# Optimization experiments

Hardware: AMD Instinct MI355X
Metric: run time of the kernel (lower is better)

## Reference

```python
import jax, jax.numpy as jnp
import numpy as np
import math

E = 64          # embed_size
S = 64          # max_seq_len (mask hard-codes seq==64)
H = 8           # num_heads
DH = E // H     # 8
DFF = 4 * E     # 256
V = 32000       # vocab_size
B = 64          # batch


def _pos_encoding():
    position = np.arange(0, S, dtype=np.float32)[:, None]
    div_term = np.exp(np.arange(0, E, 2, dtype=np.float32) * -(math.log(10000.0) / E))
    pe = np.zeros((S, E), dtype=np.float32)
    pe[:, 0::2] = np.sin(position * div_term)
    pe[:, 1::2] = np.cos(position * div_term)
    return jnp.asarray(pe)


def layernorm(x, g, b, eps=1e-5):
    mu = jnp.mean(x, -1, keepdims=True)
    var = jnp.mean((x - mu) ** 2, -1, keepdims=True)
    return (x - mu) * jax.lax.rsqrt(var + eps) * g + b


def round4(x):
    return jnp.round(x * 1e4) / 1e4


def setup_inputs() -> dict:
    key = jax.random.key(0)
    ks = jax.random.split(key, 16)
    n = lambda k, sh, s=0.05: jax.random.normal(k, sh, dtype=jnp.float32) * s
    return {
        "x": jax.random.randint(ks[0], (B, S), 0, V),
        "emb": n(ks[1], (V, E), 1.0),
        "pe": _pos_encoding(),
        # per-head q/k/v weights concatenated: [E, H*DH] == [E, E], no bias
        "wq": n(ks[2], (E, E)), "wk": n(ks[3], (E, E)), "wv": n(ks[4], (E, E)),
        "g_h": jnp.ones((E,)), "b_h": jnp.zeros((E,)),           # MHA internal LayerNorm
        "wo": n(ks[5], (E, E)), "bo": jnp.zeros((E,)),           # MHA output linear
        "g1": jnp.ones((E,)), "bt1": jnp.zeros((E,)),            # norm1
        "w1": n(ks[6], (E, DFF)), "b1f": jnp.zeros((DFF,)),      # ffn fc1
        "w2": n(ks[7], (DFF, E)), "b2f": jnp.zeros((E,)),        # ffn fc2
        "g2": jnp.ones((E,)), "bt2": jnp.zeros((E,)),            # norm2
        "gf": jnp.ones((E,)), "bf": jnp.zeros((E,)),             # final norm
        "wout": n(ks[8], (E, V)), "bout": jnp.zeros((V,)),       # final linear
    }


def reference(x, emb, pe, wq, wk, wv, g_h, b_h, wo, bo, g1, bt1,
              w1, b1f, w2, b2f, g2, bt2, gf, bf, wout, bout):
    # embedding + positional encoding (dropout = identity in eval)
    h = emb[x] + pe[:S]                              # [B,S,E]

    # --- multi-head attention (per-head linears fused as one GEMM each) ---
    q = (h @ wq).reshape(B, S, H, DH)
    k = (h @ wk).reshape(B, S, H, DH)
    v = (h @ wv).reshape(B, S, H, DH)
    scores = jnp.einsum('bshd,bthd->bhst', q, k) / math.sqrt(DH)
    causal = jnp.tril(jnp.ones((S, S), dtype=bool))
    scores = jnp.where(causal, scores, -jnp.inf)
    attn = jax.nn.softmax(scores, axis=-1)
    ho = round4(jnp.einsum('bhst,bthd->bshd', attn, v))  # per-head round(decimals=4)
    concat = ho.reshape(B, S, E)
    attn_out = jnp.round(layernorm(concat, g_h, b_h) @ wo + bo)  # round to integers

    # --- transformer block residual/norm/ffn ---
    h = layernorm(h + attn_out, g1, bt1)
    ffn = jax.nn.relu(h @ w1 + b1f) @ w2 + b2f
    h = round4(layernorm(h + ffn, g2, bt2))

    # --- final norm, vocab projection, softmax, round ---
    logits = layernorm(h, gf, bf) @ wout + bout       # [B,S,V]
    probs = jax.nn.softmax(logits, axis=-1)
    return jnp.round(probs)
```

## Files before the change

kernel.cpp:

```cpp
#include <hip/hip_runtime.h>
#include <hip/hip_bf16.h>
#include <math.h>

#define EMB 64
#define SEQ 64
#define NH 8
#define DFF 256
#define VOC 32000
#define BATCH 64

using bf16_t = __hip_bfloat16;
typedef __bf16 bf16x8 __attribute__((ext_vector_type(8)));
typedef float f32x4 __attribute__((ext_vector_type(4)));

#define WOUTT_OFF 0
#define HBF_OFF   4194304
#define GSUM_OFF  (4194304 + 524288)
#define GMAX_OFF  (GSUM_OFF + 16384)
#define H_OFF     (GMAX_OFF + 32768)
#define Q_OFF     (H_OFF + 1048576)
#define K_OFF     (Q_OFF + 1048576)
#define V_OFF     (K_OFF + 1048576)
#define HO_OFF    (V_OFF + 1048576)

#define NV_TOTAL 32768000
#define F1_BLKS 360
#define F1_PER  32000
#define F2_BLKS 192
#define F2_PER  30000
#define F3_BLKS 360
#define F3_PER  32000
#define F4_BLKS 64
#define F4_PER  62000
#define F2_BASE 11520000
#define F3_BASE 17280000
#define F4_BASE 28800000

__device__ inline void fill_slice(float* __restrict__ outp, size_t vbase, int count, int t) {
  f32x4 z = {0.f, 0.f, 0.f, 0.f};
  f32x4* o4 = (f32x4*)outp + vbase;
  for (int i = t; i < count; i += 256) o4[i] = z;
}

__device__ inline unsigned long long packmax(float f, int i) {
  unsigned u = __float_as_uint(f);
  u = (u & 0x80000000u) ? ~u : (u | 0x80000000u);
  return ((unsigned long long)u << 32) | (unsigned)i;
}

__device__ inline float rsum16(float s) {
  s += __shfl_xor(s, 1, 16);
  s += __shfl_xor(s, 2, 16);
  s += __shfl_xor(s, 4, 16);
  s += __shfl_xor(s, 8, 16);
  return s;
}

__device__ inline void gemm64g(const float* __restrict__ in, const float* __restrict__ W,
                               float* __restrict__ out, int t) {
  int i = t >> 2, j0 = (t & 3) * 16;
  float acc[16];
#pragma unroll
  for (int j = 0; j < 16; ++j) acc[j] = 0.f;
#pragma unroll 2
  for (int k = 0; k < 64; ++k) {
    float a = in[i * 65 + k];
    const float4* wr = (const float4*)(W + k * 64 + j0);
    float4 w0 = wr[0], w1v = wr[1], w2v = wr[2], w3v = wr[3];
    acc[0] += a * w0.x;   acc[1] += a * w0.y;   acc[2] += a * w0.z;   acc[3] += a * w0.w;
    acc[4] += a * w1v.x;  acc[5] += a * w1v.y;  acc[6] += a * w1v.z;  acc[7] += a * w1v.w;
    acc[8] += a * w2v.x;  acc[9] += a * w2v.y;  acc[10] += a * w2v.z; acc[11] += a * w2v.w;
    acc[12] += a * w3v.x; acc[13] += a * w3v.y; acc[14] += a * w3v.z; acc[15] += a * w3v.w;
  }
#pragma unroll
  for (int j = 0; j < 16; ++j) out[(size_t)i * 64 + j0 + j] = acc[j];
}

__global__ __launch_bounds__(256) void k_qkv(
    const int* __restrict__ x, const float* __restrict__ emb, const float* __restrict__ pe,
    const float* __restrict__ wq, const float* __restrict__ wk, const float* __restrict__ wv,
    const float* __restrict__ wout, bf16_t* __restrict__ woutT,
    float* __restrict__ H, float* __restrict__ Q, float* __restrict__ K,
    float* __restrict__ V, float* __restrict__ gsums,
    unsigned long long* __restrict__ gmax, float* __restrict__ outp) {
  const int t = threadIdx.x;
  __shared__ float sm[64 * 65];

  if (blockIdx.x >= 564) {
    fill_slice(outp, (size_t)(blockIdx.x - 564) * F1_PER, F1_PER, t);
    return;
  }

  if (blockIdx.x >= 64) {
    int v0 = (blockIdx.x - 64) * 64;
    for (int idx = t; idx < 4096; idx += 256) {
      int e = idx >> 6, c = idx & 63;
      sm[e * 65 + c] = wout[(size_t)e * VOC + v0 + c];
    }
    __syncthreads();
    for (int idx = t; idx < 4096; idx += 256) {
      int c = idx >> 6, e = idx & 63;
      woutT[(size_t)(v0 + c) * 64 + e] = __float2bfloat16(sm[e * 65 + c]);
    }
    return;
  }

  const int b = blockIdx.x;
  if (t < 64) {
    gsums[b * 64 + t] = 0.f;
    gmax[b * 64 + t] = 0ULL;
  }
  for (int idx = t; idx < 4096; idx += 256) {
    int i = idx >> 6, e = idx & 63;
    int tok = x[b * 64 + i];
    float v = emb[(size_t)tok * 64 + e] + pe[i * 64 + e];
    sm[i * 65 + e] = v;
    H[((size_t)b * 64 + i) * 64 + e] = v;
  }
  __syncthreads();
  gemm64g(sm, wq, Q + (size_t)b * 4096, t);
  gemm64g(sm, wk, K + (size_t)b * 4096, t);
  gemm64g(sm, wv, V + (size_t)b * 4096, t);
}

__global__ __launch_bounds__(256) void k_attn(const float* __restrict__ Q,
                                              const float* __restrict__ K,
                                              const float* __restrict__ V,
                                              float* __restrict__ HO,
                                              float* __restrict__ outp) {
  const int t = threadIdx.x;
  if (blockIdx.x >= 64) {
    int bid = (blockIdx.x - 64) * 8 + blockIdx.y;
    fill_slice(outp, (size_t)F2_BASE + (size_t)bid * F2_PER, F2_PER, t);
    return;
  }
  const int b = blockIdx.x, h = blockIdx.y;
  __shared__ float Qh[64 * 8], Kh[64 * 8], Vh[64 * 8];
  __shared__ float SC[64 * 65];
  const size_t base = (size_t)b * 4096 + h * 8;

  for (int idx = t; idx < 512; idx += 256) {
    int i = idx >> 3, d = idx & 7;
    Qh[i * 8 + d] = Q[base + (size_t)i * 64 + d];
    Kh[i * 8 + d] = K[base + (size_t)i * 64 + d];
    Vh[i * 8 + d] = V[base + (size_t)i * 64 + d];
  }
  __syncthreads();

  const float scale = 0.35355339059327373f;
  const int i = t >> 2, jb = t & 3;
  float qv[8];
#pragma unroll
  for (int d = 0; d < 8; ++d) qv[d] = Qh[i * 8 + d];

  float sv[16];
  float m = -INFINITY;
#pragma unroll
  for (int jj = 0; jj < 16; ++jj) {
    int j = jb * 16 + jj;
    float s;
    if (j <= i) {
      s = 0.f;
#pragma unroll
      for (int d = 0; d < 8; ++d) s += qv[d] * Kh[j * 8 + d];
      s *= scale;
    } else {
      s = -INFINITY;
    }
    sv[jj] = s;
    m = fmaxf(m, s);
  }
  m = fmaxf(m, __shfl_xor(m, 1, 4));
  m = fmaxf(m, __shfl_xor(m, 2, 4));
  float sum = 0.f;
#pragma unroll
  for (int jj = 0; jj < 16; ++jj) {
    float e2 = __expf(sv[jj] - m);
    sv[jj] = e2;
    sum += e2;
  }
  sum += __shfl_xor(sum, 1, 4);
  sum += __shfl_xor(sum, 2, 4);
  float inv = 1.f / sum;
#pragma unroll
  for (int jj = 0; jj < 16; ++jj) SC[i * 65 + jb * 16 + jj] = sv[jj] * inv;
  __syncthreads();

  for (int idx = t; idx < 512; idx += 256) {
    int ii = idx >> 3, d = idx & 7;
    float o = 0.f;
    for (int j = 0; j < 64; ++j) o += SC[ii * 65 + j] * Vh[j * 8 + d];
    HO[base + (size_t)ii * 64 + d] = rintf(o * 1e4f) / 1e4f;
  }
}

__global__ __launch_bounds__(256) void k_ffn(
    const float* __restrict__ H, const float* __restrict__ HO,
    const float* __restrict__ g_h, const float* __restrict__ b_h,
    const float* __restrict__ wo, const float* __restrict__ bo,
    const float* __restrict__ g1, const float* __restrict__ bt1,
    const float* __restrict__ w1, const float* __restrict__ b1f,
    const float* __restrict__ w2, const float* __restrict__ b2f,
    const float* __restrict__ g2, const float* __restrict__ bt2,
    const float* __restrict__ gf, const float* __restrict__ bf_,
    bf16_t* __restrict__ hbf, float* __restrict__ outp) {
  const int t = threadIdx.x;
  if (blockIdx.x >= 256) {
    fill_slice(outp, (size_t)F3_BASE + (size_t)(blockIdx.x - 256) * F3_PER, F3_PER, t);
    return;
  }
  const int r0 = blockIdx.x * 16;
  const int i = t >> 4, l = t & 15;
  const int e0 = l * 4;
  const size_t row = (size_t)(r0 + i) * 64;
  __shared__ float T1[16 * 65];
  __shared__ float T2[16 * 65];
  __shared__ float H1[16 * 65];
  __shared__ float M[16 * 260];

  {
    float4 hv = *(const float4*)(HO + row + e0);
    float mu = rsum16(hv.x + hv.y + hv.z + hv.w) * (1.f / 64.f);
    float d0 = hv.x - mu, d1 = hv.y - mu, d2 = hv.z - mu, d3 = hv.w - mu;
    float var = rsum16(d0 * d0 + d1 * d1 + d2 * d2 + d3 * d3) * (1.f / 64.f);
    float rs = rsqrtf(var + 1e-5f);
    T1[i * 65 + e0 + 0] = d0 * rs * g_h[e0 + 0] + b_h[e0 + 0];
    T1[i * 65 + e0 + 1] = d1 * rs * g_h[e0 + 1] + b_h[e0 + 1];
    T1[i * 65 + e0 + 2] = d2 * rs * g_h[e0 + 2] + b_h[e0 + 2];
    T1[i * 65 + e0 + 3] = d3 * rs * g_h[e0 + 3] + b_h[e0 + 3];
  }
  __syncthreads();

  {
    float a0 = 0.f, a1 = 0.f, a2 = 0.f, a3 = 0.f;
#pragma unroll 4
    for (int k = 0; k < 64; ++k) {
      float a = T1[i * 65 + k];
      float4 w = *(const float4*)(wo + (size_t)k * 64 + e0);
      a0 += a * w.x; a1 += a * w.y; a2 += a * w.z; a3 += a * w.w;
    }
    T2[i * 65 + e0 + 0] = rintf(a0 + bo[e0 + 0]);
    T2[i * 65 + e0 + 1] = rintf(a1 + bo[e0 + 1]);
    T2[i * 65 + e0 + 2] = rintf(a2 + bo[e0 + 2]);
    T2[i * 65 + e0 + 3] = rintf(a3 + bo[e0 + 3]);
  }
  __syncthreads();

  {
    float4 hh = *(const float4*)(H + row + e0);
    float x0 = hh.x + T2[i * 65 + e0 + 0];
    float x1 = hh.y + T2[i * 65 + e0 + 1];
    float x2 = hh.z + T2[i * 65 + e0 + 2];
    float x3 = hh.w + T2[i * 65 + e0 + 3];
    float mu = rsum16(x0 + x1 + x2 + x3) * (1.f / 64.f);
    float d0 = x0 - mu, d1 = x1 - mu, d2 = x2 - mu, d3 = x3 - mu;
    float var = rsum16(d0 * d0 + d1 * d1 + d2 * d2 + d3 * d3) * (1.f / 64.f);
    float rs = rsqrtf(var + 1e-5f);
    H1[i * 65 + e0 + 0] = d0 * rs * g1[e0 + 0] + bt1[e0 + 0];
    H1[i * 65 + e0 + 1] = d1 * rs * g1[e0 + 1] + bt1[e0 + 1];
    H1[i * 65 + e0 + 2] = d2 * rs * g1[e0 + 2] + bt1[e0 + 2];
    H1[i * 65 + e0 + 3] = d3 * rs * g1[e0 + 3] + bt1[e0 + 3];
  }
  __syncthreads();

  {
    const int j0 = l * 16;
    float acc[16];
#pragma unroll
    for (int j = 0; j < 16; ++j) acc[j] = 0.f;
#pragma unroll 2
    for (int k = 0; k < 64; ++k) {
      float a = H1[i * 65 + k];
      const float4* wr = (const float4*)(w1 + (size_t)k * 256 + j0);
      float4 w0 = wr[0], w1v = wr[1], w2v = wr[2], w3v = wr[3];
      acc[0] += a * w0.x;   acc[1] += a * w0.y;   acc[2] += a * w0.z;   acc[3] += a * w0.w;
      acc[4] += a * w1v.x;  acc[5] += a * w1v.y;  acc[6] += a * w1v.z;  acc[7] += a * w1v.w;
      acc[8] += a * w2v.x;  acc[9] += a * w2v.y;  acc[10] += a * w2v.z; acc[11] += a * w2v.w;
      acc[12] += a * w3v.x; acc[13] += a * w3v.y; acc[14] += a * w3v.z; acc[15] += a * w3v.w;
    }
#pragma unroll
    for (int j = 0; j < 16; ++j)
      M[i * 260 + j0 + j] = fmaxf(acc[j] + b1f[j0 + j], 0.f);
  }
  __syncthreads();

  float f0 = 0.f, f1 = 0.f, f2 = 0.f, f3 = 0.f;
  {
#pragma unroll 4
    for (int k = 0; k < 256; ++k) {
      float a = M[i * 260 + k];
      float4 w = *(const float4*)(w2 + (size_t)k * 64 + e0);
      f0 += a * w.x; f1 += a * w.y; f2 += a * w.z; f3 += a * w.w;
    }
    f0 += b2f[e0 + 0]; f1 += b2f[e0 + 1]; f2 += b2f[e0 + 2]; f3 += b2f[e0 + 3];
  }

  {
    float y0 = H1[i * 65 + e0 + 0] + f0;
    float y1 = H1[i * 65 + e0 + 1] + f1;
    float y2 = H1[i * 65 + e0 + 2] + f2;
    float y3 = H1[i * 65 + e0 + 3] + f3;
    float mu = rsum16(y0 + y1 + y2 + y3) * (1.f / 64.f);
    float d0 = y0 - mu, d1 = y1 - mu, d2 = y2 - mu, d3 = y3 - mu;
    float var = rsum16(d0 * d0 + d1 * d1 + d2 * d2 + d3 * d3) * (1.f / 64.f);
    float rs = rsqrtf(var + 1e-5f);
    float h20 = rintf((d0 * rs * g2[e0 + 0] + bt2[e0 + 0]) * 1e4f) / 1e4f;
    float h21 = rintf((d1 * rs * g2[e0 + 1] + bt2[e0 + 1]) * 1e4f) / 1e4f;
    float h22 = rintf((d2 * rs * g2[e0 + 2] + bt2[e0 + 2]) * 1e4f) / 1e4f;
    float h23 = rintf((d3 * rs * g2[e0 + 3] + bt2[e0 + 3]) * 1e4f) / 1e4f;
    float mu2 = rsum16(h20 + h21 + h22 + h23) * (1.f / 64.f);
    float e0d = h20 - mu2, e1d = h21 - mu2, e2d = h22 - mu2, e3d = h23 - mu2;
    float var2 = rsum16(e0d * e0d + e1d * e1d + e2d * e2d + e3d * e3d) * (1.f / 64.f);
    float rs2 = rsqrtf(var2 + 1e-5f);
    hbf[row + e0 + 0] = __float2bfloat16(e0d * rs2 * gf[e0 + 0] + bf_[e0 + 0]);
    hbf[row + e0 + 1] = __float2bfloat16(e1d * rs2 * gf[e0 + 1] + bf_[e0 + 1]);
    hbf[row + e0 + 2] = __float2bfloat16(e2d * rs2 * gf[e0 + 2] + bf_[e0 + 2]);
    hbf[row + e0 + 3] = __float2bfloat16(e3d * rs2 * gf[e0 + 3] + bf_[e0 + 3]);
  }
}

__global__ __launch_bounds__(256) void k_sumexp(const bf16_t* __restrict__ hbf,
                                                const bf16_t* __restrict__ woutT,
                                                const float* __restrict__ bout,
                                                float* __restrict__ gsums,
                                                unsigned long long* __restrict__ gmax,
                                                float* __restrict__ outp) {
  const int t = threadIdx.x;
  if (blockIdx.x >= 64) {
    int bid = (blockIdx.x - 64) * 8 + blockIdx.y;
    fill_slice(outp, (size_t)F4_BASE + (size_t)bid * F4_PER, F4_PER, t);
    return;
  }
  const int lane = t & 63, wave = t >> 6;
  const int row0 = blockIdx.x * 64;
  const int nbase = blockIdx.y * 4000;
  const int mrow = lane & 15, quad = lane >> 4;
  __shared__ float lsum[64];
  if (t < 64) lsum[t] = 0.f;
  __syncthreads();

  bf16x8 a0[4], a1[4];
#pragma unroll
  for (int at = 0; at < 4; ++at) {
    const bf16_t* arow = hbf + (size_t)(row0 + at * 16 + mrow) * 64 + quad * 8;
    a0[at] = *(const bf16x8*)(arow);
    a1[at] = *(const bf16x8*)(arow + 32);
  }

  float s[4][4];
  float mxv[4][4];
  int mxi[4][4];
#pragma unroll
  for (int at = 0; at < 4; ++at)
#pragma unroll
    for (int r = 0; r < 4; ++r) { s[at][r] = 0.f; mxv[at][r] = -INFINITY; mxi[at][r] = 0; }

  for (int tt = wave; tt < 250; tt += 4) {
    int col = nbase + tt * 16 + mrow;
    const bf16_t* brow = woutT + (size_t)col * 64 + quad * 8;
    bf16x8 b0 = *(const bf16x8*)(brow);
    bf16x8 b1 = *(const bf16x8*)(brow + 32);
    float bv = bout[col];
#pragma unroll
    for (int at = 0; at < 4; ++at) {
      f32x4 c = {0.f, 0.f, 0.f, 0.f};
      c = __builtin_amdgcn_mfma_f32_16x16x32_bf16(a0[at], b0, c, 0, 0, 0);
      c = __builtin_amdgcn_mfma_f32_16x16x32_bf16(a1[at], b1, c, 0, 0, 0);
#pragma unroll
      for (int r = 0; r < 4; ++r) {
        float v = c[r] + bv;
        s[at][r] += __expf(v);
        mxi[at][r] = (v > mxv[at][r]) ? col : mxi[at][r];
        mxv[at][r] = fmaxf(mxv[at][r], v);
      }
    }
  }
#pragma unroll
  for (int off = 1; off < 16; off <<= 1) {
#pragma unroll
    for (int at = 0; at < 4; ++at)
#pragma unroll
      for (int r = 0; r < 4; ++r) {
        s[at][r] += __shfl_xor(s[at][r], off, 64);
        float ov = __shfl_xor(mxv[at][r], off, 64);
        int oi = __shfl_xor(mxi[at][r], off, 64);
        if (ov > mxv[at][r] || (ov == mxv[at][r] && oi > mxi[at][r])) {
          mxv[at][r] = ov; mxi[at][r] = oi;
        }
      }
  }
  if (mrow == 0) {
#pragma unroll
    for (int at = 0; at < 4; ++at)
#pragma unroll
      for (int r = 0; r < 4; ++r) {
        atomicAdd(&lsum[at * 16 + quad * 4 + r], s[at][r]);
        atomicMax(&gmax[row0 + at * 16 + quad * 4 + r], packmax(mxv[at][r], mxi[at][r]));
      }
  }
  __syncthreads();
  if (t < 64) atomicAdd(&gsums[row0 + t], lsum[t]);
}

__global__ __launch_bounds__(256) void k_scatter(const float* __restrict__ gsums,
                                                 const unsigned long long* __restrict__ gmax,
                                                 float* __restrict__ out) {
  int row = blockIdx.x * 256 + threadIdx.x;
  if (row >= BATCH * SEQ) return;
  unsigned long long p = gmax[row];
  unsigned key = (unsigned)(p >> 32);
  int idx = (int)(p & 0xffffffffu);
  unsigned ub = (key & 0x80000000u) ? (key & 0x7fffffffu) : ~key;
  float lmax = __uint_as_float(ub);
  float iv = 1.0f / gsums[row];
  float v = rintf(__expf(lmax) * iv);
  if (v != 0.0f) out[(size_t)row * VOC + idx] = v;
}

extern "C" void kernel_launch(void* const* d_in, const int* in_sizes, int n_in,
                              void* d_out, int out_size, void* d_ws, size_t ws_size,
                              hipStream_t stream) {
  const int* x = (const int*)d_in[0];
  const float* emb = (const float*)d_in[1];
  const float* pe = (const float*)d_in[2];
  const float* wq = (const float*)d_in[3];
  const float* wk = (const float*)d_in[4];
  const float* wv = (const float*)d_in[5];
  const float* g_h = (const float*)d_in[6];
  const float* b_h = (const float*)d_in[7];
  const float* wo = (const float*)d_in[8];
  const float* bo = (const float*)d_in[9];
  const float* g1 = (const float*)d_in[10];
  const float* bt1 = (const float*)d_in[11];
  const float* w1 = (const float*)d_in[12];
  const float* b1f = (const float*)d_in[13];
  const float* w2 = (const float*)d_in[14];
  const float* b2f = (const float*)d_in[15];
  const float* g2 = (const float*)d_in[16];
  const float* bt2 = (const float*)d_in[17];
  const float* gf = (const float*)d_in[18];
  const float* bff = (const float*)d_in[19];
  const float* wout = (const float*)d_in[20];
  const float* bout = (const float*)d_in[21];

  char* ws = (char*)d_ws;
  bf16_t* woutT = (bf16_t*)(ws + WOUTT_OFF);
  bf16_t* hbf = (bf16_t*)(ws + HBF_OFF);
  float* gsums = (float*)(ws + GSUM_OFF);
  unsigned long long* gmax = (unsigned long long*)(ws + GMAX_OFF);
  float* H = (float*)(ws + H_OFF);
  float* Q = (float*)(ws + Q_OFF);
  float* K = (float*)(ws + K_OFF);
  float* V = (float*)(ws + V_OFF);
  float* HO = (float*)(ws + HO_OFF);
  float* out = (float*)d_out;

  k_qkv<<<564 + F1_BLKS, 256, 0, stream>>>(x, emb, pe, wq, wk, wv, wout, woutT,
                                           H, Q, K, V, gsums, gmax, out);
  k_attn<<<dim3(64 + F2_BLKS / 8, 8), 256, 0, stream>>>(Q, K, V, HO, out);
  k_ffn<<<256 + F3_BLKS, 256, 0, stream>>>(H, HO, g_h, b_h, wo, bo, g1, bt1, w1, b1f,
                                           w2, b2f, g2, bt2, gf, bff, hbf, out);
  dim3 grid(64 + F4_BLKS / 8, 8);
  k_sumexp<<<grid, 256, 0, stream>>>(hbf, woutT, bout, gsums, gmax, out);
  k_scatter<<<16, 256, 0, stream>>>(gsums, gmax, out);
}
```

Baseline: 756.9 us.

## Fuse scatter into sumexp via last-block counter and rebalance zero-fill

Removes the separate k_scatter launch. Each row-group now keeps an atomic completion counter, and the eighth block to finish reads the global sums and max and writes the rounded result. The zero-fill of the output is also taken out of k_sumexp and spread across the k_qkv and k_ffn fill blocks. This saves one kernel launch and shortens the tail of the final kernel, at the cost of extra fence and atomic traffic and heavier fill work in the earlier kernels.

```diff
diff --git a/kernel.cpp b/kernel.cpp
--- a/kernel.cpp
+++ b/kernel.cpp
@@ -17,24 +17,21 @@
 #define HBF_OFF   4194304
 #define GSUM_OFF  (4194304 + 524288)
 #define GMAX_OFF  (GSUM_OFF + 16384)
-#define H_OFF     (GMAX_OFF + 32768)
+#define DONE_OFF  (GMAX_OFF + 32768)
+#define H_OFF     (DONE_OFF + 256)
 #define Q_OFF     (H_OFF + 1048576)
 #define K_OFF     (Q_OFF + 1048576)
 #define V_OFF     (K_OFF + 1048576)
 #define HO_OFF    (V_OFF + 1048576)
 
-#define NV_TOTAL 32768000
-#define F1_BLKS 360
+#define F1_BLKS 500
 #define F1_PER  32000
 #define F2_BLKS 192
 #define F2_PER  30000
-#define F3_BLKS 360
+#define F3_BLKS 344
 #define F3_PER  32000
-#define F4_BLKS 64
-#define F4_PER  62000
-#define F2_BASE 11520000
-#define F3_BASE 17280000
-#define F4_BASE 28800000
+#define F2_BASE 16000000
+#define F3_BASE 21760000
 
 __device__ inline void fill_slice(float* __restrict__ outp, size_t vbase, int count, int t) {
   f32x4 z = {0.f, 0.f, 0.f, 0.f};
@@ -82,7 +79,8 @@
     const float* __restrict__ wout, bf16_t* __restrict__ woutT,
     float* __restrict__ H, float* __restrict__ Q, float* __restrict__ K,
     float* __restrict__ V, float* __restrict__ gsums,
-    unsigned long long* __restrict__ gmax, float* __restrict__ outp) {
+    unsigned long long* __restrict__ gmax, unsigned* __restrict__ done,
+    float* __restrict__ outp) {
   const int t = threadIdx.x;
   __shared__ float sm[64 * 65];
 
@@ -110,6 +108,7 @@
     gsums[b * 64 + t] = 0.f;
     gmax[b * 64 + t] = 0ULL;
   }
+  if (t == 0) done[b] = 0u;
   for (int idx = t; idx < 4096; idx += 256) {
     int i = idx >> 6, e = idx & 63;
     int tok = x[b * 64 + i];
@@ -324,18 +323,15 @@
                                                 const float* __restrict__ bout,
                                                 float* __restrict__ gsums,
                                                 unsigned long long* __restrict__ gmax,
-                                                float* __restrict__ outp) {
+                                                unsigned* __restrict__ done,
+                                                float* __restrict__ out) {
   const int t = threadIdx.x;
-  if (blockIdx.x >= 64) {
-    int bid = (blockIdx.x - 64) * 8 + blockIdx.y;
-    fill_slice(outp, (size_t)F4_BASE + (size_t)bid * F4_PER, F4_PER, t);
-    return;
-  }
   const int lane = t & 63, wave = t >> 6;
   const int row0 = blockIdx.x * 64;
   const int nbase = blockIdx.y * 4000;
   const int mrow = lane & 15, quad = lane >> 4;
   __shared__ float lsum[64];
+  __shared__ unsigned sdone;
   if (t < 64) lsum[t] = 0.f;
   __syncthreads();
 
@@ -400,21 +396,26 @@
   }
   __syncthreads();
   if (t < 64) atomicAdd(&gsums[row0 + t], lsum[t]);
-}
-
-__global__ __launch_bounds__(256) void k_scatter(const float* __restrict__ gsums,
-                                                 const unsigned long long* __restrict__ gmax,
-                                                 float* __restrict__ out) {
-  int row = blockIdx.x * 256 + threadIdx.x;
-  if (row >= BATCH * SEQ) return;
-  unsigned long long p = gmax[row];
-  unsigned key = (unsigned)(p >> 32);
-  int idx = (int)(p & 0xffffffffu);
-  unsigned ub = (key & 0x80000000u) ? (key & 0x7fffffffu) : ~key;
-  float lmax = __uint_as_float(ub);
-  float iv = 1.0f / gsums[row];
-  float v = rintf(__expf(lmax) * iv);
-  if (v != 0.0f) out[(size_t)row * VOC + idx] = v;
+
+  __threadfence();
+  __syncthreads();
+  if (t == 0) sdone = atomicAdd(&done[blockIdx.x], 1u);
+  __syncthreads();
+  if (sdone == 7) {
+    __threadfence();
+    if (t < 64) {
+      int row = row0 + t;
+      float sum = atomicAdd(&gsums[row], 0.f);
+      unsigned long long p = atomicAdd(&gmax[row], 0ULL);
+      unsigned key = (unsigned)(p >> 32);
+      int idx = (int)(p & 0xffffffffu);
+      unsigned ub = (key & 0x80000000u) ? (key & 0x7fffffffu) : ~key;
+      float lmax = __uint_as_float(ub);
+      float iv = 1.0f / sum;
+      float v = rintf(__expf(lmax) * iv);
+      if (v != 0.0f) out[(size_t)row * VOC + idx] = v;
+    }
+  }
 }
 
 extern "C" void kernel_launch(void* const* d_in, const int* in_sizes, int n_in,
@@ -448,6 +449,7 @@
   bf16_t* hbf = (bf16_t*)(ws + HBF_OFF);
   float* gsums = (float*)(ws + GSUM_OFF);
   unsigned long long* gmax = (unsigned long long*)(ws + GMAX_OFF);
+  unsigned* done = (unsigned*)(ws + DONE_OFF);
   float* H = (float*)(ws + H_OFF);
   float* Q = (float*)(ws + Q_OFF);
   float* K = (float*)(ws + K_OFF);
@@ -456,11 +458,9 @@
   float* out = (float*)d_out;
 
   k_qkv<<<564 + F1_BLKS, 256, 0, stream>>>(x, emb, pe, wq, wk, wv, wout, woutT,
-                                           H, Q, K, V, gsums, gmax, out);
+                                           H, Q, K, V, gsums, gmax, done, out);
   k_attn<<<dim3(64 + F2_BLKS / 8, 8), 256, 0, stream>>>(Q, K, V, HO, out);
   k_ffn<<<256 + F3_BLKS, 256, 0, stream>>>(H, HO, g_h, b_h, wo, bo, g1, bt1, w1, b1f,
                                            w2, b2f, g2, bt2, gf, bff, hbf, out);
-  dim3 grid(64 + F4_BLKS / 8, 8);
-  k_sumexp<<<grid, 256, 0, stream>>>(hbf, woutT, bout, gsums, gmax, out);
-  k_scatter<<<16, 256, 0, stream>>>(gsums, gmax, out);
-}
+  k_sumexp<<<dim3(64, 8), 256, 0, stream>>>(hbf, woutT, bout, gsums, gmax, done, out);
+}
```

Result: slower. 791.5 us (+4.6%).
